# Performance work log

Hardware: AMD Instinct MI355X
Metric: run time of the kernel (lower is better)

Reference implementation:

```python
import jax, jax.numpy as jnp
import numpy as np

D_IN = 128
D_HID = 256


def _mlp(x, W1, b1, W2, b2):
    # two-layer MLP with ReLU (dropout is identity at eval)
    h = jax.nn.relu(x @ W1 + b1)
    return jax.nn.relu(h @ W2 + b2)


def setup_inputs() -> dict:
    key = jax.random.key(0)
    kA, kB, k1, k2, k3, k4 = jax.random.split(key, 6)
    A = jax.random.normal(kA, (4, 4096, D_IN), dtype=jnp.float32)
    B = jax.random.normal(kB, (4, 4096, D_IN), dtype=jnp.float32)
    s1 = 1.0 / np.sqrt(D_IN)
    s2 = 1.0 / np.sqrt(D_HID)
    W1 = jax.random.uniform(k1, (D_IN, D_HID), jnp.float32, -s1, s1)
    b1 = jax.random.uniform(k2, (D_HID,), jnp.float32, -s1, s1)
    W2 = jax.random.uniform(k3, (D_HID, D_HID), jnp.float32, -s2, s2)
    b2 = jax.random.uniform(k4, (D_HID,), jnp.float32, -s2, s2)
    return {"A": A, "B": B, "W1": W1, "b1": b1, "W2": W2, "b2": b2}


def reference(A, B, W1, b1, W2, b2):
    f_A = _mlp(A, W1, b1, W2, b2)  # [b, m, h]
    f_B = _mlp(B, W1, b1, W2, b2)  # [b, n, h]
    e = jnp.einsum('bmh,bnh->bmn', f_A, f_B)  # unscaled scores
    beta = jnp.einsum('bmn,bnd->bmd', jax.nn.softmax(e, axis=-1), B)
    alpha = jnp.einsum('bmn,bmd->bnd', jax.nn.softmax(e, axis=-2), A)
    return (beta, alpha)
```

## Files before the change

kernel.cpp:

```cpp
#include <hip/hip_runtime.h>

typedef __attribute__((ext_vector_type(8))) short bf16x8;
typedef __attribute__((ext_vector_type(4))) float f32x4;
typedef __attribute__((ext_vector_type(16))) float f32x16;

__device__ __forceinline__ ushort f2bf(float x) {
  union { float f; unsigned u; } c; c.f = x;
  unsigned u = c.u;
  u += 0x7fffu + ((u >> 16) & 1u);
  return (ushort)(u >> 16);
}

__device__ __forceinline__ unsigned cvt_pk_bf16(float lo, float hi) {
  unsigned r;
  asm("v_cvt_pk_bf16_f32 %0, %1, %2" : "=v"(r) : "v"(lo), "v"(hi));
  return r;
}

__device__ __forceinline__ void gl_lds16(const void* g, void* s) {
  __builtin_amdgcn_global_load_lds(
      (const __attribute__((address_space(1))) unsigned*)g,
      (__attribute__((address_space(3))) unsigned*)s, 16, 0, 0);
}

__global__ __launch_bounds__(256) void prep_transpose(
    const float* __restrict__ A, const float* __restrict__ Bm,
    ushort* __restrict__ At, ushort* __restrict__ Bt)
{
  int tensor = blockIdx.z & 1, b = blockIdx.z >> 1;
  const float* in = tensor ? Bm : A;
  ushort* out = tensor ? Bt : At;
  int m0 = blockIdx.x * 64, d0 = blockIdx.y * 64;
  __shared__ ushort tile[64][72];
  int tid = threadIdx.x;
#pragma unroll
  for (int it = 0; it < 4; ++it) {
    int lin = it * 256 + tid;
    int r = lin >> 4, c4 = (lin & 15) * 4;
    const float* p = in + ((size_t)b * 4096 + m0 + r) * 128 + d0 + c4;
    float4 v = *(const float4*)p;
    tile[r][c4 + 0] = f2bf(v.x); tile[r][c4 + 1] = f2bf(v.y);
    tile[r][c4 + 2] = f2bf(v.z); tile[r][c4 + 3] = f2bf(v.w);
  }
  __syncthreads();
#pragma unroll
  for (int it = 0; it < 2; ++it) {
    int lin = it * 256 + tid;
    int dr = lin >> 3, cm = (lin & 7) * 8;
    bf16x8 v;
#pragma unroll
    for (int j = 0; j < 8; ++j) v[j] = (short)tile[cm + j][dr];
    *(bf16x8*)(out + ((size_t)b * 128 + d0 + dr) * 4096 + m0 + cm) = v;
  }
}

__global__ __launch_bounds__(256) void prep_w(
    const float* __restrict__ W1, const float* __restrict__ W2,
    ushort* __restrict__ Wt1, ushort* __restrict__ Wt2)
{
  int idx = blockIdx.x * 256 + threadIdx.x;
  if (idx < 32768) {
    int k = idx >> 8, n = idx & 255;
    Wt1[n * 128 + k] = f2bf(W1[idx]);
  }
  {
    int k = idx >> 8, n = idx & 255;
    Wt2[n * 256 + k] = f2bf(W2[idx]);
  }
}

template<int KD, bool F32IN>
__global__ __launch_bounds__(256) void mlp2(
    const void* __restrict__ X0, const void* __restrict__ X1,
    const ushort* __restrict__ Wt, const float* __restrict__ bias,
    ushort* __restrict__ out0, ushort* __restrict__ out1)
{
  const void* X = blockIdx.y ? X1 : X0;
  ushort* out = blockIdx.y ? out1 : out0;
  int l = threadIdx.x & 63, w = threadIdx.x >> 6;
  int rowbase = blockIdx.x * 64 + w * 16;
  constexpr int NK = KD / 32;
  bf16x8 xf[NK];
  {
    int r = rowbase + (l & 15);
    int koff = (l >> 4) * 8;
    if (F32IN) {
      const float* Xp = (const float*)X + (size_t)r * KD + koff;
#pragma unroll
      for (int kc = 0; kc < NK; ++kc) {
        float4 a = *(const float4*)(Xp + kc * 32);
        float4 c = *(const float4*)(Xp + kc * 32 + 4);
        bf16x8 v;
        v[0] = (short)f2bf(a.x); v[1] = (short)f2bf(a.y);
        v[2] = (short)f2bf(a.z); v[3] = (short)f2bf(a.w);
        v[4] = (short)f2bf(c.x); v[5] = (short)f2bf(c.y);
        v[6] = (short)f2bf(c.z); v[7] = (short)f2bf(c.w);
        xf[kc] = v;
      }
    } else {
      const ushort* Xp = (const ushort*)X + (size_t)r * KD + koff;
#pragma unroll
      for (int kc = 0; kc < NK; ++kc) xf[kc] = *(const bf16x8*)(Xp + kc * 32);
    }
  }
  f32x4 acc[16];
#pragma unroll
  for (int i = 0; i < 16; ++i) acc[i] = (f32x4){0.f, 0.f, 0.f, 0.f};
#pragma unroll
  for (int kc = 0; kc < NK; ++kc) {
#pragma unroll
    for (int nf = 0; nf < 16; ++nf) {
      bf16x8 bfv = *(const bf16x8*)&Wt[(size_t)(nf * 16 + (l & 15)) * KD + kc * 32 + (l >> 4) * 8];
      acc[nf] = __builtin_amdgcn_mfma_f32_16x16x32_bf16(xf[kc], bfv, acc[nf], 0, 0, 0);
    }
  }
#pragma unroll
  for (int nf = 0; nf < 16; ++nf) {
    int col = nf * 16 + (l & 15);
    float bv = bias[col];
#pragma unroll
    for (int i = 0; i < 4; ++i) {
      float v = acc[nf][i] + bv;
      v = fmaxf(v, 0.f);
      out[(size_t)(rowbase + (l >> 4) * 4 + i) * 256 + col] = f2bf(v);
    }
  }
}

__global__ __launch_bounds__(256, 2) void flash2(
    const ushort* __restrict__ fA, const ushort* __restrict__ fB,
    const ushort* __restrict__ At, const ushort* __restrict__ Bt,
    float* __restrict__ out)
{
  int bp = blockIdx.x;
  int pass = bp >> 2, b = bp & 3;
  int qbase = blockIdx.y * 64;
  const ushort* fQ = pass ? fB : fA;
  const ushort* fK = pass ? fA : fB;
  const ushort* Vg = pass ? At : Bt;
  float* O = out + (size_t)pass * (4u * 4096 * 128) + (size_t)b * 4096 * 128;

  __shared__ ushort Kl[2][64 * 256];

  int tid = threadIdx.x;
  int l = tid & 63, w = tid >> 6;
  int l31 = l & 31, g5 = l >> 5;
  int qw = w & 1, kw = w >> 1;

  const size_t fkbase = (size_t)b * 4096 * 256;
  const size_t vgbase = (size_t)b * 128 * 4096;

  auto stage_k = [&](int t_, int buf_) {
    const ushort* kp = fK + fkbase + (size_t)t_ * 16384;
    ushort* lb = &Kl[buf_][0] + w * 4096;
#pragma unroll
    for (int s = 0; s < 8; ++s) {
      int row = w * 16 + s * 2 + g5;
      int gs = l31 ^ (row & 7);
      gl_lds16(kp + (size_t)row * 256 + gs * 8, lb + s * 512);
    }
  };

  bf16x8 q[16];
  {
    const ushort* qp = fQ + fkbase + (size_t)(qbase + qw * 32 + l31) * 256 + g5 * 8;
#pragma unroll
    for (int kc = 0; kc < 16; ++kc) q[kc] = *(const bf16x8*)(qp + kc * 16);
  }

  f32x16 acc_o0 = {}, acc_o1 = {}, acc_o2 = {}, acc_o3 = {};
  float m_run = -INFINITY, l_run = 0.f;

  stage_k(0, 0);

  for (int t = 0; t < 64; ++t) {
    int cur = t & 1;
    __syncthreads();
    if (t < 63) stage_k(t + 1, cur ^ 1);

    bf16x8 vv[2][4];
#pragma unroll
    for (int dblk = 0; dblk < 4; ++dblk) {
      const ushort* vp = Vg + vgbase + (size_t)(dblk * 32 + l31) * 4096
                         + t * 64 + kw * 32 + g5 * 8;
#pragma unroll
      for (int kblk = 0; kblk < 2; ++kblk)
        vv[kblk][dblk] = *(const bf16x8*)(vp + kblk * 16);
    }

    const ushort* kbuf = &Kl[cur][0];
    int krow = kw * 32 + l31;
    int sx = l31 & 7;
    f32x16 s0 = {}, s1 = {};
#pragma unroll
    for (int kc = 0; kc < 8; ++kc) {
      bf16x8 a0 = *(const bf16x8*)&kbuf[krow * 256 + (((4 * kc + g5) ^ sx) * 8)];
      bf16x8 a1 = *(const bf16x8*)&kbuf[krow * 256 + (((4 * kc + 2 + g5) ^ sx) * 8)];
      s0 = __builtin_amdgcn_mfma_f32_32x32x16_bf16(a0, q[2 * kc],     s0, 0, 0, 0);
      s1 = __builtin_amdgcn_mfma_f32_32x32x16_bf16(a1, q[2 * kc + 1], s1, 0, 0, 0);
    }

    float sv[16];
#pragma unroll
    for (int r = 0; r < 16; ++r) sv[r] = s0[r] + s1[r];

    float pmax = sv[0];
#pragma unroll
    for (int r = 1; r < 16; ++r) pmax = fmaxf(pmax, sv[r]);
    pmax = fmaxf(pmax, __shfl_xor(pmax, 32));

    if (!__all(pmax <= m_run + 8.f)) {
      float mnew = fmaxf(m_run, pmax);
      float sc = __expf(m_run - mnew);
      l_run *= sc;
#pragma unroll
      for (int r = 0; r < 16; ++r) {
        float scr = __shfl(sc, (r & 3) + 8 * (r >> 2) + 4 * g5);
        acc_o0[r] *= scr; acc_o1[r] *= scr; acc_o2[r] *= scr; acc_o3[r] *= scr;
      }
      m_run = mnew;
    }

    float p[16], psum = 0.f;
#pragma unroll
    for (int r = 0; r < 16; ++r) {
      p[r] = __expf(sv[r] - m_run);
      psum += p[r];
    }
    l_run += psum + __shfl_xor(psum, 32);

    unsigned pk[4][2];
#pragma unroll
    for (int r2 = 0; r2 < 4; ++r2) {
      pk[r2][0] = cvt_pk_bf16(p[4 * r2 + 0], p[4 * r2 + 1]);
      pk[r2][1] = cvt_pk_bf16(p[4 * r2 + 2], p[4 * r2 + 3]);
    }

#pragma unroll
    for (int kblk = 0; kblk < 2; ++kblk) {
      int r2a = 2 * kblk, r2b = r2a + 1;
      unsigned la0 = pk[r2a][0], la1 = pk[r2a][1];
      unsigned lb0 = pk[r2b][0], lb1 = pk[r2b][1];
      unsigned s0w = g5 ? la0 : lb0, s1w = g5 ? la1 : lb1;
      unsigned rc0 = (unsigned)__shfl_xor((int)s0w, 32);
      unsigned rc1 = (unsigned)__shfl_xor((int)s1w, 32);
      union { unsigned u[4]; bf16x8 v; } pf;
      pf.u[0] = g5 ? rc0 : la0;  pf.u[1] = g5 ? rc1 : la1;
      pf.u[2] = g5 ? lb0 : rc0;  pf.u[3] = g5 ? lb1 : rc1;
      acc_o0 = __builtin_amdgcn_mfma_f32_32x32x16_bf16(pf.v, vv[kblk][0], acc_o0, 0, 0, 0);
      acc_o1 = __builtin_amdgcn_mfma_f32_32x32x16_bf16(pf.v, vv[kblk][1], acc_o1, 0, 0, 0);
      acc_o2 = __builtin_amdgcn_mfma_f32_32x32x16_bf16(pf.v, vv[kblk][2], acc_o2, 0, 0, 0);
      acc_o3 = __builtin_amdgcn_mfma_f32_32x32x16_bf16(pf.v, vv[kblk][3], acc_o3, 0, 0, 0);
    }
  }

  __syncthreads();
  float* shm = (float*)&Kl[0][0];
  shm[w * 128 + l] = m_run;
  shm[w * 128 + 64 + l] = l_run;
  {
    float* sa = shm + 512 + w * 2048;
    const f32x16& send0 = kw ? acc_o0 : acc_o2;
    const f32x16& send1 = kw ? acc_o1 : acc_o3;
#pragma unroll
    for (int r = 0; r < 16; ++r) {
      sa[r * 64 + l] = send0[r];
      sa[1024 + r * 64 + l] = send1[r];
    }
  }
  __syncthreads();
  {
    int pw = w ^ 2;
    float m1 = shm[pw * 128 + l];
    float l1 = shm[pw * 128 + 64 + l];
    float M = fmaxf(m_run, m1);
    float a0 = __expf(m_run - M), a1 = __expf(m1 - M);
    float inv = 1.f / (l_run * a0 + l1 * a1);
    const float* sp = shm + 512 + pw * 2048;
    const f32x16& keep0 = kw ? acc_o2 : acc_o0;
    const f32x16& keep1 = kw ? acc_o3 : acc_o1;
    int dbase = kw ? 64 : 0;
    int qr = qbase + qw * 32;
#pragma unroll
    for (int r = 0; r < 16; ++r) {
      int rowl = (r & 3) + 8 * (r >> 2) + 4 * g5;
      float invr = __shfl(inv, rowl);
      float a0r = __shfl(a0, rowl);
      float a1r = __shfl(a1, rowl);
      float* op = O + (size_t)(qr + rowl) * 128 + dbase + l31;
      op[0]  = (keep0[r] * a0r + sp[r * 64 + l] * a1r) * invr;
      op[32] = (keep1[r] * a0r + sp[1024 + r * 64 + l] * a1r) * invr;
    }
  }
}

extern "C" void kernel_launch(void* const* d_in, const int* in_sizes, int n_in,
                              void* d_out, int out_size, void* d_ws, size_t ws_size,
                              hipStream_t stream) {
  const float* A  = (const float*)d_in[0];
  const float* Bm = (const float*)d_in[1];
  const float* W1 = (const float*)d_in[2];
  const float* b1 = (const float*)d_in[3];
  const float* W2 = (const float*)d_in[4];
  const float* b2 = (const float*)d_in[5];
  float* out = (float*)d_out;

  ushort* ws = (ushort*)d_ws;
  ushort* hA  = ws;
  ushort* hB  = hA + 4194304;
  ushort* fA  = hB + 4194304;
  ushort* fB  = fA + 4194304;
  ushort* At  = fB + 4194304;
  ushort* Bt  = At + 2097152;
  ushort* Wt1 = Bt + 2097152;
  ushort* Wt2 = Wt1 + 32768;

  prep_transpose<<<dim3(64, 2, 8), 256, 0, stream>>>(A, Bm, At, Bt);
  prep_w<<<256, 256, 0, stream>>>(W1, W2, Wt1, Wt2);
  mlp2<128, true ><<<dim3(256, 2), 256, 0, stream>>>(A, Bm, Wt1, b1, hA, hB);
  mlp2<256, false><<<dim3(256, 2), 256, 0, stream>>>(hA, hB, Wt2, b2, fA, fB);
  flash2<<<dim3(8, 64), 256, 0, stream>>>(fA, fB, At, Bt, out);
}
```

Before: 237.4 us.

## Prefetch V one tile ahead, widen LDS swizzle, add sched barriers and priorities

The flash-attention loop is unrolled by two so V register fragments are double-buffered and loaded one tile ahead, alongside the K LDS staging. The loop uses explicit waitcnt with s_barrier, sched_barrier fences and s_setprio around the MFMA groups. It also widens the K LDS XOR swizzle from 3 to 5 bits to cut bank conflicts, and turns the max and sum reductions into trees. The cost is higher register pressure from the second V buffer under launch_bounds(256,2), plus a hand-written vmcnt that depends on the exact load count.

```diff
diff --git a/kernel.cpp b/kernel.cpp
--- a/kernel.cpp
+++ b/kernel.cpp
@@ -127,7 +127,7 @@
   }
 }
 
-__global__ __launch_bounds__(256, 2) void flash2(
+__global__ __launch_bounds__(256, 2) void flash5(
     const ushort* __restrict__ fA, const ushort* __restrict__ fB,
     const ushort* __restrict__ At, const ushort* __restrict__ Bt,
     float* __restrict__ out)
@@ -156,8 +156,18 @@
 #pragma unroll
     for (int s = 0; s < 8; ++s) {
       int row = w * 16 + s * 2 + g5;
-      int gs = l31 ^ (row & 7);
+      int gs = l31 ^ (row & 31);
       gl_lds16(kp + (size_t)row * 256 + gs * 8, lb + s * 512);
+    }
+  };
+
+  auto loadV = [&](bf16x8 (&vn)[2][4], int t_) {
+#pragma unroll
+    for (int dblk = 0; dblk < 4; ++dblk) {
+      const ushort* vp = Vg + vgbase + (size_t)(dblk * 32 + l31) * 4096
+                         + t_ * 64 + kw * 32 + g5 * 8;
+      vn[0][dblk] = *(const bf16x8*)(vp);
+      vn[1][dblk] = *(const bf16x8*)(vp + 16);
     }
   };
 
@@ -171,43 +181,50 @@
   f32x16 acc_o0 = {}, acc_o1 = {}, acc_o2 = {}, acc_o3 = {};
   float m_run = -INFINITY, l_run = 0.f;
 
+  bf16x8 vvA[2][4], vvB[2][4];
+
   stage_k(0, 0);
-
-  for (int t = 0; t < 64; ++t) {
-    int cur = t & 1;
-    __syncthreads();
-    if (t < 63) stage_k(t + 1, cur ^ 1);
-
-    bf16x8 vv[2][4];
-#pragma unroll
-    for (int dblk = 0; dblk < 4; ++dblk) {
-      const ushort* vp = Vg + vgbase + (size_t)(dblk * 32 + l31) * 4096
-                         + t * 64 + kw * 32 + g5 * 8;
-#pragma unroll
-      for (int kblk = 0; kblk < 2; ++kblk)
-        vv[kblk][dblk] = *(const bf16x8*)(vp + kblk * 16);
-    }
-
-    const ushort* kbuf = &Kl[cur][0];
+  __builtin_amdgcn_sched_barrier(0);
+  loadV(vvA, 0);
+  __builtin_amdgcn_sched_barrier(0);
+
+  auto subiter = [&](int t, int cb, bf16x8 (&vc)[2][4], bf16x8 (&vn)[2][4]) {
+    __builtin_amdgcn_sched_barrier(0);
+    asm volatile("s_waitcnt lgkmcnt(0) vmcnt(8)" ::: "memory");
+    __builtin_amdgcn_s_barrier();
+    __builtin_amdgcn_sched_barrier(0);
+    if (t < 63) {
+      stage_k(t + 1, cb ^ 1);
+      __builtin_amdgcn_sched_barrier(0);
+      loadV(vn, t + 1);
+      __builtin_amdgcn_sched_barrier(0);
+    }
+
+    const ushort* kbuf = &Kl[cb][0];
     int krow = kw * 32 + l31;
-    int sx = l31 & 7;
     f32x16 s0 = {}, s1 = {};
+    __builtin_amdgcn_s_setprio(1);
 #pragma unroll
     for (int kc = 0; kc < 8; ++kc) {
-      bf16x8 a0 = *(const bf16x8*)&kbuf[krow * 256 + (((4 * kc + g5) ^ sx) * 8)];
-      bf16x8 a1 = *(const bf16x8*)&kbuf[krow * 256 + (((4 * kc + 2 + g5) ^ sx) * 8)];
+      bf16x8 a0 = *(const bf16x8*)&kbuf[krow * 256 + (((4 * kc + g5)     ^ l31) * 8)];
+      bf16x8 a1 = *(const bf16x8*)&kbuf[krow * 256 + (((4 * kc + 2 + g5) ^ l31) * 8)];
       s0 = __builtin_amdgcn_mfma_f32_32x32x16_bf16(a0, q[2 * kc],     s0, 0, 0, 0);
       s1 = __builtin_amdgcn_mfma_f32_32x32x16_bf16(a1, q[2 * kc + 1], s1, 0, 0, 0);
     }
+    __builtin_amdgcn_s_setprio(0);
 
     float sv[16];
 #pragma unroll
     for (int r = 0; r < 16; ++r) sv[r] = s0[r] + s1[r];
 
-    float pmax = sv[0];
-#pragma unroll
-    for (int r = 1; r < 16; ++r) pmax = fmaxf(pmax, sv[r]);
-    pmax = fmaxf(pmax, __shfl_xor(pmax, 32));
+    float mx[16];
+#pragma unroll
+    for (int r = 0; r < 16; ++r) mx[r] = sv[r];
+#pragma unroll
+    for (int off = 8; off >= 1; off >>= 1)
+#pragma unroll
+      for (int r = 0; r < off; ++r) mx[r] = fmaxf(mx[r], mx[r + off]);
+    float pmax = fmaxf(mx[0], __shfl_xor(mx[0], 32));
 
     if (!__all(pmax <= m_run + 8.f)) {
       float mnew = fmaxf(m_run, pmax);
@@ -221,13 +238,17 @@
       m_run = mnew;
     }
 
-    float p[16], psum = 0.f;
-#pragma unroll
-    for (int r = 0; r < 16; ++r) {
-      p[r] = __expf(sv[r] - m_run);
-      psum += p[r];
-    }
-    l_run += psum + __shfl_xor(psum, 32);
+    float p[16];
+#pragma unroll
+    for (int r = 0; r < 16; ++r) p[r] = __expf(sv[r] - m_run);
+    float ps[16];
+#pragma unroll
+    for (int r = 0; r < 16; ++r) ps[r] = p[r];
+#pragma unroll
+    for (int off = 8; off >= 1; off >>= 1)
+#pragma unroll
+      for (int r = 0; r < off; ++r) ps[r] += ps[r + off];
+    l_run += ps[0] + __shfl_xor(ps[0], 32);
 
     unsigned pk[4][2];
 #pragma unroll
@@ -247,11 +268,18 @@
       union { unsigned u[4]; bf16x8 v; } pf;
       pf.u[0] = g5 ? rc0 : la0;  pf.u[1] = g5 ? rc1 : la1;
       pf.u[2] = g5 ? lb0 : rc0;  pf.u[3] = g5 ? lb1 : rc1;
-      acc_o0 = __builtin_amdgcn_mfma_f32_32x32x16_bf16(pf.v, vv[kblk][0], acc_o0, 0, 0, 0);
-      acc_o1 = __builtin_amdgcn_mfma_f32_32x32x16_bf16(pf.v, vv[kblk][1], acc_o1, 0, 0, 0);
-      acc_o2 = __builtin_amdgcn_mfma_f32_32x32x16_bf16(pf.v, vv[kblk][2], acc_o2, 0, 0, 0);
-      acc_o3 = __builtin_amdgcn_mfma_f32_32x32x16_bf16(pf.v, vv[kblk][3], acc_o3, 0, 0, 0);
-    }
+      __builtin_amdgcn_s_setprio(1);
+      acc_o0 = __builtin_amdgcn_mfma_f32_32x32x16_bf16(pf.v, vc[kblk][0], acc_o0, 0, 0, 0);
+      acc_o1 = __builtin_amdgcn_mfma_f32_32x32x16_bf16(pf.v, vc[kblk][1], acc_o1, 0, 0, 0);
+      acc_o2 = __builtin_amdgcn_mfma_f32_32x32x16_bf16(pf.v, vc[kblk][2], acc_o2, 0, 0, 0);
+      acc_o3 = __builtin_amdgcn_mfma_f32_32x32x16_bf16(pf.v, vc[kblk][3], acc_o3, 0, 0, 0);
+      __builtin_amdgcn_s_setprio(0);
+    }
+  };
+
+  for (int t2 = 0; t2 < 32; ++t2) {
+    subiter(2 * t2,     0, vvA, vvB);
+    subiter(2 * t2 + 1, 1, vvB, vvA);
   }
 
   __syncthreads();
@@ -319,5 +347,5 @@
   prep_w<<<256, 256, 0, stream>>>(W1, W2, Wt1, Wt2);
   mlp2<128, true ><<<dim3(256, 2), 256, 0, stream>>>(A, Bm, Wt1, b1, hA, hB);
   mlp2<256, false><<<dim3(256, 2), 256, 0, stream>>>(hA, hB, Wt2, b2, fA, fB);
-  flash2<<<dim3(8, 64), 256, 0, stream>>>(fA, fB, At, Bt, out);
-}
+  flash5<<<dim3(8, 64), 256, 0, stream>>>(fA, fB, At, Bt, out);
+}
```

Result: slower. 305.8 us (+28.8%).

## Fuse both MLP layers and input transpose into one kernel

Applied to the files above, without the earlier changes.

Merges the two MLP GEMM kernels into a single kernel. The hidden activation now goes through LDS instead of a global bf16 buffer. The bf16 transpose of A/B, formerly a separate prep kernel, is also folded in, using the bf16 tile already staged in LDS. This removes two kernel launches and a global round trip of the hidden tensor and a second read of the fp32 inputs, at the cost of more LDS per block and possibly lower occupancy.

```diff
diff --git a/kernel.cpp b/kernel.cpp
--- a/kernel.cpp
+++ b/kernel.cpp
@@ -21,37 +21,6 @@
   __builtin_amdgcn_global_load_lds(
       (const __attribute__((address_space(1))) unsigned*)g,
       (__attribute__((address_space(3))) unsigned*)s, 16, 0, 0);
-}
-
-__global__ __launch_bounds__(256) void prep_transpose(
-    const float* __restrict__ A, const float* __restrict__ Bm,
-    ushort* __restrict__ At, ushort* __restrict__ Bt)
-{
-  int tensor = blockIdx.z & 1, b = blockIdx.z >> 1;
-  const float* in = tensor ? Bm : A;
-  ushort* out = tensor ? Bt : At;
-  int m0 = blockIdx.x * 64, d0 = blockIdx.y * 64;
-  __shared__ ushort tile[64][72];
-  int tid = threadIdx.x;
-#pragma unroll
-  for (int it = 0; it < 4; ++it) {
-    int lin = it * 256 + tid;
-    int r = lin >> 4, c4 = (lin & 15) * 4;
-    const float* p = in + ((size_t)b * 4096 + m0 + r) * 128 + d0 + c4;
-    float4 v = *(const float4*)p;
-    tile[r][c4 + 0] = f2bf(v.x); tile[r][c4 + 1] = f2bf(v.y);
-    tile[r][c4 + 2] = f2bf(v.z); tile[r][c4 + 3] = f2bf(v.w);
-  }
-  __syncthreads();
-#pragma unroll
-  for (int it = 0; it < 2; ++it) {
-    int lin = it * 256 + tid;
-    int dr = lin >> 3, cm = (lin & 7) * 8;
-    bf16x8 v;
-#pragma unroll
-    for (int j = 0; j < 8; ++j) v[j] = (short)tile[cm + j][dr];
-    *(bf16x8*)(out + ((size_t)b * 128 + d0 + dr) * 4096 + m0 + cm) = v;
-  }
 }
 
 __global__ __launch_bounds__(256) void prep_w(
@@ -69,60 +38,108 @@
   }
 }
 
-template<int KD, bool F32IN>
-__global__ __launch_bounds__(256) void mlp2(
-    const void* __restrict__ X0, const void* __restrict__ X1,
-    const ushort* __restrict__ Wt, const float* __restrict__ bias,
-    ushort* __restrict__ out0, ushort* __restrict__ out1)
+__global__ __launch_bounds__(256) void fused_mlp(
+    const float* __restrict__ A, const float* __restrict__ Bm,
+    const ushort* __restrict__ Wt1, const float* __restrict__ b1,
+    const ushort* __restrict__ Wt2, const float* __restrict__ b2,
+    ushort* __restrict__ fA, ushort* __restrict__ fB,
+    ushort* __restrict__ At, ushort* __restrict__ Bt)
 {
-  const void* X = blockIdx.y ? X1 : X0;
-  ushort* out = blockIdx.y ? out1 : out0;
-  int l = threadIdx.x & 63, w = threadIdx.x >> 6;
+  const float* X = blockIdx.y ? Bm : A;
+  ushort* outF = blockIdx.y ? fB : fA;
+  ushort* outT = blockIdx.y ? Bt : At;
+
+  __shared__ ushort Xl[64][136];
+  __shared__ ushort Hl[64][264];
+
+  int tid = threadIdx.x;
+  int l = tid & 63, w = tid >> 6;
   int rowbase = blockIdx.x * 64 + w * 16;
-  constexpr int NK = KD / 32;
-  bf16x8 xf[NK];
+
+  bf16x8 xf[4];
   {
     int r = rowbase + (l & 15);
     int koff = (l >> 4) * 8;
-    if (F32IN) {
-      const float* Xp = (const float*)X + (size_t)r * KD + koff;
-#pragma unroll
-      for (int kc = 0; kc < NK; ++kc) {
-        float4 a = *(const float4*)(Xp + kc * 32);
-        float4 c = *(const float4*)(Xp + kc * 32 + 4);
-        bf16x8 v;
-        v[0] = (short)f2bf(a.x); v[1] = (short)f2bf(a.y);
-        v[2] = (short)f2bf(a.z); v[3] = (short)f2bf(a.w);
-        v[4] = (short)f2bf(c.x); v[5] = (short)f2bf(c.y);
-        v[6] = (short)f2bf(c.z); v[7] = (short)f2bf(c.w);
-        xf[kc] = v;
-      }
-    } else {
-      const ushort* Xp = (const ushort*)X + (size_t)r * KD + koff;
-#pragma unroll
-      for (int kc = 0; kc < NK; ++kc) xf[kc] = *(const bf16x8*)(Xp + kc * 32);
-    }
-  }
-  f32x4 acc[16];
-#pragma unroll
-  for (int i = 0; i < 16; ++i) acc[i] = (f32x4){0.f, 0.f, 0.f, 0.f};
-#pragma unroll
-  for (int kc = 0; kc < NK; ++kc) {
+    const float* Xp = X + (size_t)r * 128 + koff;
+#pragma unroll
+    for (int kc = 0; kc < 4; ++kc) {
+      float4 a = *(const float4*)(Xp + kc * 32);
+      float4 c = *(const float4*)(Xp + kc * 32 + 4);
+      bf16x8 v;
+      v[0] = (short)f2bf(a.x); v[1] = (short)f2bf(a.y);
+      v[2] = (short)f2bf(a.z); v[3] = (short)f2bf(a.w);
+      v[4] = (short)f2bf(c.x); v[5] = (short)f2bf(c.y);
+      v[6] = (short)f2bf(c.z); v[7] = (short)f2bf(c.w);
+      xf[kc] = v;
+      *(bf16x8*)&Xl[w * 16 + (l & 15)][koff + kc * 32] = v;
+    }
+  }
+
+  f32x4 acc1[16];
+#pragma unroll
+  for (int i = 0; i < 16; ++i) acc1[i] = (f32x4){0.f, 0.f, 0.f, 0.f};
+#pragma unroll
+  for (int kc = 0; kc < 4; ++kc) {
 #pragma unroll
     for (int nf = 0; nf < 16; ++nf) {
-      bf16x8 bfv = *(const bf16x8*)&Wt[(size_t)(nf * 16 + (l & 15)) * KD + kc * 32 + (l >> 4) * 8];
-      acc[nf] = __builtin_amdgcn_mfma_f32_16x16x32_bf16(xf[kc], bfv, acc[nf], 0, 0, 0);
-    }
-  }
+      bf16x8 bfv = *(const bf16x8*)&Wt1[(size_t)(nf * 16 + (l & 15)) * 128 + kc * 32 + (l >> 4) * 8];
+      acc1[nf] = __builtin_amdgcn_mfma_f32_16x16x32_bf16(xf[kc], bfv, acc1[nf], 0, 0, 0);
+    }
+  }
+  __syncthreads();
+
+  {
+    int b = (blockIdx.x * 64) >> 12;
+    int m0 = (blockIdx.x * 64) & 4095;
+    int d = tid >> 1, mh = (tid & 1) * 32;
+    ushort* op = outT + ((size_t)b * 128 + d) * 4096 + m0 + mh;
+#pragma unroll
+    for (int g = 0; g < 4; ++g) {
+      bf16x8 v;
+#pragma unroll
+      for (int j = 0; j < 8; ++j) v[j] = (short)Xl[mh + g * 8 + j][d];
+      *(bf16x8*)(op + g * 8) = v;
+    }
+  }
+
 #pragma unroll
   for (int nf = 0; nf < 16; ++nf) {
     int col = nf * 16 + (l & 15);
-    float bv = bias[col];
+    float bv = b1[col];
 #pragma unroll
     for (int i = 0; i < 4; ++i) {
-      float v = acc[nf][i] + bv;
-      v = fmaxf(v, 0.f);
-      out[(size_t)(rowbase + (l >> 4) * 4 + i) * 256 + col] = f2bf(v);
+      float v = fmaxf(acc1[nf][i] + bv, 0.f);
+      Hl[w * 16 + (l >> 4) * 4 + i][col] = f2bf(v);
+    }
+  }
+  __syncthreads();
+
+  bf16x8 hf[8];
+  {
+    int koff = (l >> 4) * 8;
+#pragma unroll
+    for (int kc = 0; kc < 8; ++kc)
+      hf[kc] = *(const bf16x8*)&Hl[w * 16 + (l & 15)][koff + kc * 32];
+  }
+  f32x4 acc2[16];
+#pragma unroll
+  for (int i = 0; i < 16; ++i) acc2[i] = (f32x4){0.f, 0.f, 0.f, 0.f};
+#pragma unroll
+  for (int kc = 0; kc < 8; ++kc) {
+#pragma unroll
+    for (int nf = 0; nf < 16; ++nf) {
+      bf16x8 bfv = *(const bf16x8*)&Wt2[(size_t)(nf * 16 + (l & 15)) * 256 + kc * 32 + (l >> 4) * 8];
+      acc2[nf] = __builtin_amdgcn_mfma_f32_16x16x32_bf16(hf[kc], bfv, acc2[nf], 0, 0, 0);
+    }
+  }
+#pragma unroll
+  for (int nf = 0; nf < 16; ++nf) {
+    int col = nf * 16 + (l & 15);
+    float bv = b2[col];
+#pragma unroll
+    for (int i = 0; i < 4; ++i) {
+      float v = fmaxf(acc2[nf][i] + bv, 0.f);
+      outF[(size_t)(rowbase + (l >> 4) * 4 + i) * 256 + col] = f2bf(v);
     }
   }
 }
@@ -306,18 +323,15 @@
   float* out = (float*)d_out;
 
   ushort* ws = (ushort*)d_ws;
-  ushort* hA  = ws;
-  ushort* hB  = hA + 4194304;
-  ushort* fA  = hB + 4194304;
+  ushort* fA  = ws;
   ushort* fB  = fA + 4194304;
   ushort* At  = fB + 4194304;
   ushort* Bt  = At + 2097152;
   ushort* Wt1 = Bt + 2097152;
   ushort* Wt2 = Wt1 + 32768;
 
-  prep_transpose<<<dim3(64, 2, 8), 256, 0, stream>>>(A, Bm, At, Bt);
   prep_w<<<256, 256, 0, stream>>>(W1, W2, Wt1, Wt2);
-  mlp2<128, true ><<<dim3(256, 2), 256, 0, stream>>>(A, Bm, Wt1, b1, hA, hB);
-  mlp2<256, false><<<dim3(256, 2), 256, 0, stream>>>(hA, hB, Wt2, b2, fA, fB);
+  fused_mlp<<<dim3(256, 2), 256, 0, stream>>>(A, Bm, Wt1, b1, Wt2, b2,
+                                              fA, fB, At, Bt);
   flash2<<<dim3(8, 64), 256, 0, stream>>>(fA, fB, At, Bt, out);
 }
```

After: 233.3 us, median of 3. No clear change (-1.7%).
